# Kernel optimization log

Measured on AMD Instinct MI355X. Metric: run time of the kernel, lower is better.

Reference implementation:

```python
import jax, jax.numpy as jnp
import numpy as np

B, I, H = 8192, 1024, 1024

def setup_inputs() -> dict:
    key = jax.random.key(0)
    ks = jax.random.split(key, 6)
    s_in = 1.0 / np.sqrt(I)
    s_h = 1.0 / np.sqrt(H)
    return {
        "x": jax.random.normal(ks[0], (B, I), jnp.float32),
        "h_prev": jax.random.normal(ks[1], (B, H), jnp.float32),
        "c_prev": jax.random.normal(ks[2], (B, H), jnp.float32),
        "Wx": jax.random.normal(ks[3], (4, H, I), jnp.float32) * s_in,   # gate order: input, forget, cell, output
        "Wh": jax.random.normal(ks[4], (4, H, H), jnp.float32) * s_h,
        "bh": jax.random.normal(ks[5], (4, H), jnp.float32) * s_h,
    }

def reference(x, h_prev, c_prev, Wx, Wh, bh):
    # Fused: 2 batched GEMMs for all 4 gates -> [B, 4, H]
    gates = (jnp.einsum('bi,ghi->bgh', x, Wx)
             + jnp.einsum('bk,ghk->bgh', h_prev, Wh)
             + bh[None, :, :])
    i = jax.nn.sigmoid(gates[:, 0])
    f = jax.nn.sigmoid(gates[:, 1])
    g = jnp.tanh(gates[:, 2])
    o = jax.nn.sigmoid(gates[:, 3])
    c_next = f * c_prev + i * g
    h_next = o * jnp.tanh(c_next)
    return (h_next, c_next)
```

## Files before the change

### kernel.cpp

```cpp
#include <hip/hip_runtime.h>
#include <hip/hip_bf16.h>
#include <stdint.h>

#define B_DIM 8192
#define I_DIM 1024
#define H_DIM 1024

typedef __attribute__((ext_vector_type(8))) short short8;
typedef __attribute__((ext_vector_type(4))) float f32x4;

static __device__ __forceinline__ short f2b(float f) {
    __bf16 h = (__bf16)f;
    return __builtin_bit_cast(short, h);
}

static __device__ __forceinline__ short8 pack8(float4 a, float4 b) {
    short8 s;
    s[0] = f2b(a.x); s[1] = f2b(a.y); s[2] = f2b(a.z); s[3] = f2b(a.w);
    s[4] = f2b(b.x); s[5] = f2b(b.y); s[6] = f2b(b.z); s[7] = f2b(b.w);
    return s;
}

static __device__ __forceinline__ float sigmoid_f(float x) {
    return 1.0f / (1.0f + __expf(-x));
}

static __device__ __forceinline__ float tanh_fast(float x) {
    x = fminf(fmaxf(x, -15.0f), 15.0f);
    float e = __expf(2.0f * x);
    return (e - 1.0f) / (e + 1.0f);
}

static __device__ __forceinline__ void load_lds16(const void* gptr, void* lptr) {
    __builtin_amdgcn_global_load_lds(
        (const __attribute__((address_space(1))) uint32_t*)gptr,
        (__attribute__((address_space(3))) uint32_t*)lptr, 16, 0, 0);
}

#define GA_GROUPS (512 * 32 * 2 * 64)
#define GB_GROUPS (256 * 32 * 2 * 64)

__global__ __launch_bounds__(256) void convert_kernel(
    const float* __restrict__ x, const float* __restrict__ h,
    const float* __restrict__ wx, const float* __restrict__ wh,
    short* __restrict__ Aw, short* __restrict__ Bw)
{
    const int64_t total = (int64_t)GA_GROUPS + GB_GROUPS;
    for (int64_t g = (int64_t)blockIdx.x * blockDim.x + threadIdx.x; g < total;
         g += (int64_t)gridDim.x * blockDim.x) {
        const float* src;
        short* dst;
        if (g < GA_GROUPS) {
            const int lane = (int)(g & 63);
            const int rest = (int)(g >> 6);
            const int kh   = rest & 1;
            const int tk   = (rest >> 1) & 31;
            const int mfrag = rest >> 6;
            const int row = (mfrag << 4) + (lane & 15);
            const int k   = (tk << 6) + (kh << 5) + ((lane >> 4) << 3);
            src = (k < 1024) ? (x + (size_t)row * 1024 + k)
                             : (h + (size_t)row * 1024 + (k - 1024));
            dst = Aw + (size_t)g * 8;
        } else {
            const int64_t gb = g - GA_GROUPS;
            const int lane = (int)(gb & 63);
            const int rest = (int)(gb >> 6);
            const int kh   = rest & 1;
            const int tk   = (rest >> 1) & 31;
            const int nfrag = rest >> 6;
            const int cf   = nfrag & 15;
            const int bn   = nfrag >> 4;
            const int gate = cf & 3;
            const int col  = (bn << 6) + ((cf >> 2) << 4) + (lane & 15);
            const int k    = (tk << 6) + (kh << 5) + ((lane >> 4) << 3);
            src = (k < 1024) ? (wx + ((size_t)(gate << 10) + col) * 1024 + k)
                             : (wh + ((size_t)(gate << 10) + col) * 1024 + (k - 1024));
            dst = Bw + (size_t)gb * 8;
        }
        float4 v0 = ((const float4*)src)[0];
        float4 v1 = ((const float4*)src)[1];
        *(short8*)dst = pack8(v0, v1);
    }
}

#define AOFF(d, f) ((d) * 4096 + (f) * 512)

__global__ __launch_bounds__(256, 4) void lstm_gemm_bd_kernel(
    const short* __restrict__ Aw, const short* __restrict__ Bw,
    const float* __restrict__ cprev, const float* __restrict__ bh,
    float* __restrict__ out)
{
    __shared__ __align__(16) short smem[8192];

    const int bid = blockIdx.x;
    const int xcd = bid & 7;
    const int c   = bid >> 3;
    const int bm  = c >> 2;
    const int ht  = 4 * xcd + (c & 3);
    const int m0  = bm * 128;

    const int t    = threadIdx.x;
    const int lane = t & 63;
    const int w    = t >> 6;
    const int wm   = w >> 1;
    const int wn   = w & 1;
    const int lc   = lane & 15;

    const short* aSrc0 = Aw + (size_t)(bm * 8 + 2 * w)     * 32768 + lane * 8;
    const short* aSrc1 = Aw + (size_t)(bm * 8 + 2 * w + 1) * 32768 + lane * 8;
    const short* bBase = Bw + (size_t)(ht * 8 + wn * 4) * 32768 + lane * 8;

    f32x4 acc[4][4] = {};
    short8 bvA[4], bvB[4];

    load_lds16(aSrc0, &smem[AOFF(0, 2 * w)]);
    load_lds16(aSrc1, &smem[AOFF(0, 2 * w + 1)]);
    #pragma unroll
    for (int j = 0; j < 4; ++j)
        bvA[j] = *(const short8*)(bBase + (size_t)j * 32768);
    asm volatile("s_waitcnt vmcnt(0)" ::: "memory");
    __builtin_amdgcn_s_barrier();

#define TILE(d, tp, BC, BN) do { \
    short8 av[4]; \
    _Pragma("unroll") \
    for (int i = 0; i < 4; ++i) \
        av[i] = *(const short8*)&smem[AOFF(d, wm * 4 + i) + lane * 8]; \
    load_lds16(aSrc0 + (tp) * 512, &smem[AOFF(d ^ 1, 2 * w)]); \
    load_lds16(aSrc1 + (tp) * 512, &smem[AOFF(d ^ 1, 2 * w + 1)]); \
    _Pragma("unroll") \
    for (int j = 0; j < 4; ++j) \
        BN[j] = *(const short8*)(bBase + (size_t)j * 32768 + (size_t)(tp) * 512); \
    __builtin_amdgcn_s_setprio(1); \
    _Pragma("unroll") \
    for (int i = 0; i < 4; ++i) \
        _Pragma("unroll") \
        for (int j = 0; j < 4; ++j) \
            acc[i][j] = __builtin_amdgcn_mfma_f32_16x16x32_bf16( \
                av[i], BC[j], acc[i][j], 0, 0, 0); \
    __builtin_amdgcn_s_setprio(0); \
    asm volatile("s_waitcnt vmcnt(0)" ::: "memory"); \
    __builtin_amdgcn_s_barrier(); \
} while (0)

    #pragma unroll 1
    for (int tk2 = 0; tk2 < 32; ++tk2) {
        const int t1 = 2 * tk2 + 1;
        const int t2 = (t1 + 1 < 64) ? t1 + 1 : 63;
        TILE(0, t1, bvA, bvB);
        TILE(1, t2, bvB, bvA);
    }
#undef TILE

    const int rg = lane >> 4;
    const int h  = ht * 32 + wn * 16 + lc;
    const float b_i = bh[0 * H_DIM + h];
    const float b_f = bh[1 * H_DIM + h];
    const float b_g = bh[2 * H_DIM + h];
    const float b_o = bh[3 * H_DIM + h];

    #pragma unroll
    for (int mf = 0; mf < 4; ++mf) {
        #pragma unroll
        for (int r = 0; r < 4; ++r) {
            const int row = m0 + wm * 64 + mf * 16 + rg * 4 + r;
            const float pi = acc[mf][0][r] + b_i;
            const float pf = acc[mf][1][r] + b_f;
            const float pg = acc[mf][2][r] + b_g;
            const float po = acc[mf][3][r] + b_o;
            const float iv = sigmoid_f(pi);
            const float fv = sigmoid_f(pf);
            const float gv = tanh_fast(pg);
            const float ov = sigmoid_f(po);
            const float cp = cprev[(size_t)row * H_DIM + h];
            const float cn = fv * cp + iv * gv;
            const float hn = ov * tanh_fast(cn);
            out[(size_t)row * H_DIM + h] = hn;
            out[(size_t)B_DIM * H_DIM + (size_t)row * H_DIM + h] = cn;
        }
    }
}

static __device__ __forceinline__ int swz(int row, int k) {
    int byte = (row << 7) + (k << 1);
    byte ^= (row & 7) << 4;
    return byte >> 1;
}

__global__ __launch_bounds__(256, 2) void lstm_fallback_kernel(
    const float* __restrict__ x, const float* __restrict__ hprev,
    const float* __restrict__ cprev, const float* __restrict__ Wx,
    const float* __restrict__ Wh, const float* __restrict__ bh,
    float* __restrict__ out)
{
    __shared__ __align__(16) short As[128 * 64];
    __shared__ __align__(16) short Bs[128 * 64];

    int bid = blockIdx.x;
    bid = (bid & 7) * 256 + (bid >> 3);
    const int mt = bid >> 5;
    const int ht = bid & 31;
    const int m0 = mt * 128;
    const int h0 = ht * 32;

    const int t    = threadIdx.x;
    const int lane = t & 63;
    const int w    = t >> 6;
    const int wr   = w >> 1;
    const int wc   = w & 1;

    const int srow = t >> 3;
    const int sk   = (t & 7) * 8;

    f32x4 acc[4][4] = {};

    #pragma unroll 1
    for (int phase = 0; phase < 2; ++phase) {
        const float* __restrict__ Ap = phase ? hprev : x;
        const float* __restrict__ Bp = phase ? Wh : Wx;
        #pragma unroll 1
        for (int kk = 0; kk < 1024; kk += 64) {
            __syncthreads();
            #pragma unroll
            for (int p = 0; p < 4; ++p) {
                const int row = srow + p * 32;
                const float4* src = (const float4*)(Ap + (size_t)(m0 + row) * I_DIM + kk + sk);
                *(short8*)&As[swz(row, sk)] = pack8(src[0], src[1]);
            }
            #pragma unroll
            for (int p = 0; p < 4; ++p) {
                const int n    = srow + p * 32;
                const int gate = (n >> 4) & 3;
                const int hcol = h0 + ((n >> 6) << 4) + (n & 15);
                const float4* src = (const float4*)(Bp + (size_t)((gate << 10) + hcol) * 1024 + kk + sk);
                *(short8*)&Bs[swz(n, sk)] = pack8(src[0], src[1]);
            }
            __syncthreads();
            #pragma unroll
            for (int ks = 0; ks < 2; ++ks) {
                const int kb = ks * 32 + ((lane >> 4) << 3);
                short8 a[4], b[4];
                #pragma unroll
                for (int m = 0; m < 4; ++m)
                    a[m] = *(const short8*)&As[swz(wr * 64 + m * 16 + (lane & 15), kb)];
                #pragma unroll
                for (int j = 0; j < 4; ++j)
                    b[j] = *(const short8*)&Bs[swz(wc * 64 + j * 16 + (lane & 15), kb)];
                #pragma unroll
                for (int m = 0; m < 4; ++m)
                    #pragma unroll
                    for (int j = 0; j < 4; ++j)
                        acc[m][j] = __builtin_amdgcn_mfma_f32_16x16x32_bf16(a[m], b[j], acc[m][j], 0, 0, 0);
            }
        }
    }

    const int cl = lane & 15;
    const int rg = lane >> 4;
    const int h  = h0 + wc * 16 + cl;
    const float b_i = bh[0 * H_DIM + h];
    const float b_f = bh[1 * H_DIM + h];
    const float b_g = bh[2 * H_DIM + h];
    const float b_o = bh[3 * H_DIM + h];

    #pragma unroll
    for (int m = 0; m < 4; ++m) {
        #pragma unroll
        for (int r = 0; r < 4; ++r) {
            const int row = m0 + wr * 64 + m * 16 + rg * 4 + r;
            const float pi = acc[m][0][r] + b_i;
            const float pf = acc[m][1][r] + b_f;
            const float pg = acc[m][2][r] + b_g;
            const float po = acc[m][3][r] + b_o;
            const float iv = sigmoid_f(pi);
            const float fv = sigmoid_f(pf);
            const float gv = tanh_fast(pg);
            const float ov = sigmoid_f(po);
            const float cp = cprev[(size_t)row * H_DIM + h];
            const float cn = fv * cp + iv * gv;
            const float hn = ov * tanh_fast(cn);
            out[(size_t)row * H_DIM + h] = hn;
            out[(size_t)B_DIM * H_DIM + (size_t)row * H_DIM + h] = cn;
        }
    }
}

extern "C" void kernel_launch(void* const* d_in, const int* in_sizes, int n_in,
                              void* d_out, int out_size, void* d_ws, size_t ws_size,
                              hipStream_t stream) {
    const float* x     = (const float*)d_in[0];
    const float* hprev = (const float*)d_in[1];
    const float* cprev = (const float*)d_in[2];
    const float* Wx    = (const float*)d_in[3];
    const float* Wh    = (const float*)d_in[4];
    const float* bh    = (const float*)d_in[5];
    float* out = (float*)d_out;

    const size_t need = ((size_t)B_DIM * 2048 + (size_t)4096 * 2048) * sizeof(short);
    if (ws_size >= need && d_ws != nullptr) {
        short* Aw = (short*)d_ws;
        short* Bw = Aw + (size_t)512 * 32768;
        hipLaunchKernelGGL(convert_kernel, dim3(4096), dim3(256), 0, stream,
                           x, hprev, Wx, Wh, Aw, Bw);
        hipLaunchKernelGGL(lstm_gemm_bd_kernel, dim3(2048), dim3(256), 0, stream,
                           Aw, Bw, cprev, bh, out);
    } else {
        hipLaunchKernelGGL(lstm_fallback_kernel, dim3(2048), dim3(256), 0, stream,
                           x, hprev, cprev, Wx, Wh, bh, out);
    }
}
```

Baseline: 164.1 us.

## Deepen A-tile LDS pipeline to four stages and drop per-tile vmcnt(0) wait

Replaces the double-buffered LDS staging of the A operand with a 4-slot ring that prefetches two K-tiles ahead. The explicit s_waitcnt vmcnt(0) after every tile is removed, so the compiler's own waits on the B register loads are relied on to cover the earlier-issued A loads before each barrier. The aim is to keep more global loads in flight and stop stalling on memory every tile. In exchange LDS use doubles to 32KB and launch bounds drop from 4 to 3 blocks per CU, which may lower occupancy. Correctness now depends on the in-order vmcnt counting implied by the load issue order.

```diff
diff --git a/kernel.cpp b/kernel.cpp
--- a/kernel.cpp
+++ b/kernel.cpp
@@ -83,20 +83,20 @@
     }
 }
 
-#define AOFF(d, f) ((d) * 4096 + (f) * 512)
-
-__global__ __launch_bounds__(256, 4) void lstm_gemm_bd_kernel(
+#define AOFF(r, f) ((r) * 4096 + (f) * 512)
+
+__global__ __launch_bounds__(256, 3) void lstm_gemm_hyb_kernel(
     const short* __restrict__ Aw, const short* __restrict__ Bw,
     const float* __restrict__ cprev, const float* __restrict__ bh,
     float* __restrict__ out)
 {
-    __shared__ __align__(16) short smem[8192];
+    __shared__ __align__(16) short smem[16384];
 
     const int bid = blockIdx.x;
     const int xcd = bid & 7;
     const int c   = bid >> 3;
     const int bm  = c >> 2;
-    const int ht  = 4 * xcd + (c & 3);
+    const int nt  = 4 * xcd + (c & 3);
     const int m0  = bm * 128;
 
     const int t    = threadIdx.x;
@@ -108,29 +108,27 @@
 
     const short* aSrc0 = Aw + (size_t)(bm * 8 + 2 * w)     * 32768 + lane * 8;
     const short* aSrc1 = Aw + (size_t)(bm * 8 + 2 * w + 1) * 32768 + lane * 8;
-    const short* bBase = Bw + (size_t)(ht * 8 + wn * 4) * 32768 + lane * 8;
+    const short* bBase = Bw + (size_t)(nt * 8 + wn * 4) * 32768 + lane * 8;
 
     f32x4 acc[4][4] = {};
     short8 bvA[4], bvB[4];
 
-    load_lds16(aSrc0, &smem[AOFF(0, 2 * w)]);
-    load_lds16(aSrc1, &smem[AOFF(0, 2 * w + 1)]);
-    #pragma unroll
-    for (int j = 0; j < 4; ++j)
-        bvA[j] = *(const short8*)(bBase + (size_t)j * 32768);
-    asm volatile("s_waitcnt vmcnt(0)" ::: "memory");
-    __builtin_amdgcn_s_barrier();
-
-#define TILE(d, tp, BC, BN) do { \
+#define BLOAD(BV, p) { \
+    _Pragma("unroll") \
+    for (int j = 0; j < 4; ++j) \
+        BV[j] = *(const short8*)(bBase + (size_t)j * 32768 + (size_t)(p) * 512); }
+
+#define ASTAGE(r, p) \
+    load_lds16(aSrc0 + (p) * 512, &smem[AOFF(r, 2 * w)]); \
+    load_lds16(aSrc1 + (p) * 512, &smem[AOFF(r, 2 * w + 1)]);
+
+#define TILE(r, rs, BC, BN, pa, pb) do { \
+    ASTAGE(rs, pa) \
+    BLOAD(BN, pb) \
     short8 av[4]; \
     _Pragma("unroll") \
     for (int i = 0; i < 4; ++i) \
-        av[i] = *(const short8*)&smem[AOFF(d, wm * 4 + i) + lane * 8]; \
-    load_lds16(aSrc0 + (tp) * 512, &smem[AOFF(d ^ 1, 2 * w)]); \
-    load_lds16(aSrc1 + (tp) * 512, &smem[AOFF(d ^ 1, 2 * w + 1)]); \
-    _Pragma("unroll") \
-    for (int j = 0; j < 4; ++j) \
-        BN[j] = *(const short8*)(bBase + (size_t)j * 32768 + (size_t)(tp) * 512); \
+        av[i] = *(const short8*)&smem[AOFF(r, wm * 4 + i) + lane * 8]; \
     __builtin_amdgcn_s_setprio(1); \
     _Pragma("unroll") \
     for (int i = 0; i < 4; ++i) \
@@ -139,21 +137,35 @@
             acc[i][j] = __builtin_amdgcn_mfma_f32_16x16x32_bf16( \
                 av[i], BC[j], acc[i][j], 0, 0, 0); \
     __builtin_amdgcn_s_setprio(0); \
-    asm volatile("s_waitcnt vmcnt(0)" ::: "memory"); \
     __builtin_amdgcn_s_barrier(); \
 } while (0)
 
+    ASTAGE(0, 0)
+    ASTAGE(1, 1)
+    BLOAD(bvA, 0)
+    asm volatile("s_waitcnt vmcnt(6)" ::: "memory");
+    __builtin_amdgcn_s_barrier();
+
     #pragma unroll 1
-    for (int tk2 = 0; tk2 < 32; ++tk2) {
-        const int t1 = 2 * tk2 + 1;
-        const int t2 = (t1 + 1 < 64) ? t1 + 1 : 63;
-        TILE(0, t1, bvA, bvB);
-        TILE(1, t2, bvB, bvA);
+    for (int q = 0; q < 16; ++q) {
+        const int t0 = 4 * q;
+        const int c2 = (t0 + 2 < 64) ? t0 + 2 : 63;
+        const int c3 = (t0 + 3 < 64) ? t0 + 3 : 63;
+        const int c4 = (t0 + 4 < 64) ? t0 + 4 : 63;
+        const int c5 = (t0 + 5 < 64) ? t0 + 5 : 63;
+        const int c1 = t0 + 1;
+        TILE(0, 2, bvA, bvB, c2, c1);
+        TILE(1, 3, bvB, bvA, c3, c2);
+        TILE(2, 0, bvA, bvB, c4, c3);
+        TILE(3, 1, bvB, bvA, c5, c4);
     }
 #undef TILE
+#undef ASTAGE
+#undef BLOAD
+    asm volatile("s_waitcnt vmcnt(0)" ::: "memory");
 
     const int rg = lane >> 4;
-    const int h  = ht * 32 + wn * 16 + lc;
+    const int h  = nt * 32 + wn * 16 + lc;
     const float b_i = bh[0 * H_DIM + h];
     const float b_f = bh[1 * H_DIM + h];
     const float b_g = bh[2 * H_DIM + h];
@@ -302,7 +314,7 @@
         short* Bw = Aw + (size_t)512 * 32768;
         hipLaunchKernelGGL(convert_kernel, dim3(4096), dim3(256), 0, stream,
                            x, hprev, Wx, Wh, Aw, Bw);
-        hipLaunchKernelGGL(lstm_gemm_bd_kernel, dim3(2048), dim3(256), 0, stream,
+        hipLaunchKernelGGL(lstm_gemm_hyb_kernel, dim3(2048), dim3(256), 0, stream,
                            Aw, Bw, cprev, bh, out);
     } else {
         hipLaunchKernelGGL(lstm_fallback_kernel, dim3(2048), dim3(256), 0, stream,
```

After: 164.5 us. About the same (+0.3%).
